# Kernel tuning notes

Measured on AMD Instinct MI355X. Metric: run time of the kernel, lower is better.

## Reference

```python
import jax, jax.numpy as jnp
import numpy as np

SCALE_FACTORS = (0.5, 1.0)
ITERATIONS = (2, 2)
TAU = (1.0, 1.0)
SIGMA = (1.0, 1.0)
SIGMA_CUTOFF = 3.0
EPS = 1e-9
DHW = ('NCDHW', 'OIDHW', 'NCDHW')


def gaussian_kernel1d(sigma):
    radius = int(round(sigma * SIGMA_CUTOFF))
    x = np.arange(-radius, radius + 1, dtype=np.float32)
    k = np.exp(-0.5 * (x / sigma) ** 2)
    return jnp.asarray(k / k.sum())


def smooth3d(vf, kernel):
    # separable depthwise Gaussian over the 3 spatial axes; vf: (B,C,D,H,W)
    C = vf.shape[1]
    n = kernel.shape[0]
    for axis in range(3):
        shape = [1, 1, 1]
        shape[axis] = n
        kern = jnp.broadcast_to(kernel.reshape(1, 1, *shape), (C, 1, *shape))
        vf = jax.lax.conv_general_dilated(vf, kern, (1, 1, 1), 'SAME',
                                          feature_group_count=C, dimension_numbers=DHW)
    return vf


def resize_tri(x, spatial):
    return jax.image.resize(x, x.shape[:2] + tuple(spatial), method='trilinear')


def warp(img, flow):
    # trilinear grid-sample with voxel-space displacement, border clamping
    B, C, D, H, W = img.shape
    gz, gy, gx = jnp.meshgrid(jnp.arange(D, dtype=img.dtype),
                              jnp.arange(H, dtype=img.dtype),
                              jnp.arange(W, dtype=img.dtype), indexing='ij')
    base = jnp.stack([gz, gy, gx])  # (3,D,H,W)

    def one(im, fl):
        z = jnp.clip(base[0] + fl[0], 0.0, D - 1)
        y = jnp.clip(base[1] + fl[1], 0.0, H - 1)
        x = jnp.clip(base[2] + fl[2], 0.0, W - 1)
        z0 = jnp.floor(z); y0 = jnp.floor(y); x0 = jnp.floor(x)
        wz = z - z0; wy = y - y0; wx = x - x0
        z0i = z0.astype(jnp.int32); y0i = y0.astype(jnp.int32); x0i = x0.astype(jnp.int32)
        z1i = jnp.minimum(z0i + 1, D - 1)
        y1i = jnp.minimum(y0i + 1, H - 1)
        x1i = jnp.minimum(x0i + 1, W - 1)

        def g(zi, yi, xi):
            return im[:, zi, yi, xi]  # (C,D,H,W)

        return (g(z0i, y0i, x0i) * (1 - wz) * (1 - wy) * (1 - wx)
                + g(z0i, y0i, x1i) * (1 - wz) * (1 - wy) * wx
                + g(z0i, y1i, x0i) * (1 - wz) * wy * (1 - wx)
                + g(z0i, y1i, x1i) * (1 - wz) * wy * wx
                + g(z1i, y0i, x0i) * wz * (1 - wy) * (1 - wx)
                + g(z1i, y0i, x1i) * wz * (1 - wy) * wx
                + g(z1i, y1i, x0i) * wz * wy * (1 - wx)
                + g(z1i, y1i, x1i) * wz * wy * wx)

    return jax.vmap(one)(img, flow)


def demon_forces(warped, fixed):
    # 'active' demon forces: gradient of the warped moving image
    diff = warped - fixed                                  # (B,1,D,H,W)
    g = jnp.stack(jnp.gradient(warped[:, 0], axis=(1, 2, 3)), axis=1)  # (B,3,D,H,W)
    denom = jnp.sum(g * g, axis=1, keepdims=True) + diff * diff + EPS
    return diff * g / denom


def conv3(x, w, b=None):
    y = jax.lax.conv_general_dilated(x, w, (1, 1, 1), 'SAME', dimension_numbers=DHW)
    return y if b is None else y + b.reshape(1, -1, 1, 1, 1)


def inorm(x):  # InstanceNorm3d, affine=False, eps=1e-5
    m = x.mean(axis=(2, 3, 4), keepdims=True)
    v = x.var(axis=(2, 3, 4), keepdims=True)
    return (x - m) * jax.lax.rsqrt(v + 1e-5)


def mish(x):
    return x * jnp.tanh(jax.nn.softplus(x))


def updater(x, w1, w2, w3, w4, b4):
    x = mish(inorm(conv3(x, w1)))
    x = mish(inorm(conv3(x, w2)))
    x = mish(inorm(conv3(x, w3)))
    return conv3(x, w4, b4)


def match_vf(vf, spatial):
    old = vf.shape[2:]
    if tuple(old) == tuple(spatial):
        return vf
    vf2 = resize_tri(vf, spatial)
    scale = jnp.array([s1 / s2 for s1, s2 in zip(spatial, old)], dtype=vf.dtype)
    return vf2 * scale.reshape(1, 3, 1, 1, 1)


def registration(image, moving, w1, w2, w3, w4, b4):
    vf = None
    for i, (sf, iters) in enumerate(zip(SCALE_FACTORS, ITERATIONS)):
        spatial = tuple(int(s * sf) for s in image.shape[2:])
        si = resize_tri(image, spatial)
        smov = resize_tri(moving, spatial)
        vf = jnp.zeros((image.shape[0], 3) + spatial, image.dtype) if vf is None else match_vf(vf, spatial)
        kernel = gaussian_kernel1d(SIGMA[i]).astype(image.dtype)
        for _ in range(iters):
            warped = warp(smov, vf)
            forces = demon_forces(warped, si)
            feat = jnp.concatenate([forces, si, warped], axis=1)  # 5 channels
            vf = vf + TAU[i] * updater(feat, w1, w2, w3, w4, b4)
            vf = smooth3d(vf, kernel)
    vf = match_vf(vf, image.shape[2:])
    warped_full = warp(moving, vf)
    return warped_full, vf


def setup_inputs() -> dict:
    key = jax.random.key(0)
    ks = jax.random.split(key, 8)
    D = H = W = 96
    return {
        'image': jax.random.uniform(ks[0], (1, 1, D, H, W), jnp.float32),
        'mask': jnp.ones((1, 1, D, H, W), jnp.float32),
        'moving': jax.random.uniform(ks[1], (1, 1, D, H, W), jnp.float32),
        'spacing': jnp.ones((3,), jnp.float32),
        'w1': jax.random.normal(ks[2], (32, 5, 3, 3, 3), jnp.float32) * 0.05,
        'w2': jax.random.normal(ks[3], (64, 32, 3, 3, 3), jnp.float32) * 0.05,
        'w3': jax.random.normal(ks[4], (32, 64, 3, 3, 3), jnp.float32) * 0.05,
        'w4': jax.random.normal(ks[5], (3, 32, 3, 3, 3), jnp.float32) * 0.05,
        'b4': jnp.zeros((3,), jnp.float32),
    }


def reference(image, mask, moving, spacing, w1, w2, w3, w4, b4):
    # mask only feeds metrics/early-stopping (disabled: early_stopping_fn='none');
    # spacing unused since use_image_spacing=False.
    return registration(image, moving, w1, w2, w3, w4, b4)
```

## Files before the change

### kernel.cpp

```cpp
#include <hip/hip_runtime.h>
#include <hip/hip_bf16.h>


#define DEV __device__ __forceinline__
typedef __hip_bfloat16 bf16;
typedef __attribute__((ext_vector_type(8))) short short8;
typedef __attribute__((ext_vector_type(4))) float f32x4;

DEV float bfu(unsigned int u) {
  union { unsigned int i; float f; } x; x.i = u << 16; return x.f;
}
DEV unsigned short fbf(float f) {
  __hip_bfloat16 h = __float2bfloat16(f);
  return __builtin_bit_cast(unsigned short, h);
}

DEV float mishf(float v) {
  if (v > 20.f) return v;
  float u = __expf(v);
  float w = u * (u + 2.f);
  return v * (w / (w + 2.f));
}

__global__ void zero_k(float* __restrict__ p, int n) {
  int i = blockIdx.x * 256 + threadIdx.x;
  if (i < n) p[i] = 0.f;
}
__global__ void copy_k(const float* __restrict__ in, float* __restrict__ out, int n) {
  int i = blockIdx.x * 256 + threadIdx.x;
  if (i < n) out[i] = in[i];
}

__global__ void pack_wf_k(const float* __restrict__ w, bf16* __restrict__ dst,
                          int NWT, int KB, int COR, int CIR) {
  int idx = blockIdx.x * 256 + threadIdx.x;
  int tot = 27 * NWT * KB * 512;
  if (idx >= tot) return;
  int j = idx & 7;
  int lane = (idx >> 3) & 63;
  int frag = idx >> 9;
  int kb = frag % KB;
  int r2 = frag / KB;
  int nwt = r2 % NWT;
  int off = r2 / NWT;
  int co = nwt * 16 + (lane & 15);
  int ci = (kb * 4 + (lane >> 4)) * 8 + j;
  float v = (co < COR && ci < CIR) ? w[((size_t)co * CIR + ci) * 27 + off] : 0.f;
  dst[idx] = __float2bfloat16(v);
}

DEV int ds_taps(int i, int n_out, int* j0, float* w) {
  if (i == 0) { *j0 = 0; w[0] = 3.f/7.f; w[1] = 3.f/7.f; w[2] = 1.f/7.f; return 3; }
  if (i == n_out - 1) { *j0 = 2*i - 1; w[0] = 1.f/7.f; w[1] = 3.f/7.f; w[2] = 3.f/7.f; return 3; }
  *j0 = 2*i - 1; w[0] = 0.125f; w[1] = 0.375f; w[2] = 0.375f; w[3] = 0.125f; return 4;
}
DEV void up_taps(int i, int n_in, int* j0, int* j1, float* w0, float* w1) {
  if (i & 1) {
    int k = i >> 1;
    if (k + 1 >= n_in) { *j0 = n_in - 1; *j1 = n_in - 1; *w0 = 1.f; *w1 = 0.f; }
    else { *j0 = k; *j1 = k + 1; *w0 = 0.75f; *w1 = 0.25f; }
  } else {
    int k = i >> 1;
    if (k == 0) { *j0 = 0; *j1 = 0; *w0 = 1.f; *w1 = 0.f; }
    else { *j0 = k - 1; *j1 = k; *w0 = 0.25f; *w1 = 0.75f; }
  }
}

__global__ void down2x_k(const float* __restrict__ in, float* __restrict__ out,
                         int Do, int Ho, int Wo) {
  const int Hi = 2 * Ho, Wi = 2 * Wo;
  const int No = Do * Ho * Wo;
  int i = blockIdx.x * 256 + threadIdx.x;
  if (i >= No) return;
  int xo = i % Wo; int t = i / Wo; int yo = t % Ho; int zo = t / Ho;
  int jz0, jy0, jx0; float wz[4], wy[4], wx[4];
  int cz = ds_taps(zo, Do, &jz0, wz);
  int cy = ds_taps(yo, Ho, &jy0, wy);
  int cx = ds_taps(xo, Wo, &jx0, wx);
  float s = 0.f;
  for (int a = 0; a < cz; ++a) {
    const float* pz = in + (size_t)(jz0 + a) * Hi * Wi;
    for (int b = 0; b < cy; ++b) {
      const float* py = pz + (size_t)(jy0 + b) * Wi;
      float wab = wz[a] * wy[b];
      for (int d = 0; d < cx; ++d) s += wab * wx[d] * py[jx0 + d];
    }
  }
  out[i] = s;
}

__global__ void up2x_vf_k(const float* __restrict__ in, float* __restrict__ out,
                          int Do, int Ho, int Wo) {
  const int Di = Do / 2, Hi = Ho / 2, Wi = Wo / 2;
  const int No = Do * Ho * Wo;
  const int c = blockIdx.y;
  int i = blockIdx.x * 256 + threadIdx.x;
  if (i >= No) return;
  int xo = i % Wo; int t = i / Wo; int yo = t % Ho; int zo = t / Ho;
  int jz0, jz1, jy0, jy1, jx0, jx1; float wz0, wz1, wy0, wy1, wx0, wx1;
  up_taps(zo, Di, &jz0, &jz1, &wz0, &wz1);
  up_taps(yo, Hi, &jy0, &jy1, &wy0, &wy1);
  up_taps(xo, Wi, &jx0, &jx1, &wx0, &wx1);
  const float* p = in + (size_t)c * Di * Hi * Wi;
  float v00 = wx0 * p[(jz0 * Hi + jy0) * Wi + jx0] + wx1 * p[(jz0 * Hi + jy0) * Wi + jx1];
  float v01 = wx0 * p[(jz0 * Hi + jy1) * Wi + jx0] + wx1 * p[(jz0 * Hi + jy1) * Wi + jx1];
  float v10 = wx0 * p[(jz1 * Hi + jy0) * Wi + jx0] + wx1 * p[(jz1 * Hi + jy0) * Wi + jx1];
  float v11 = wx0 * p[(jz1 * Hi + jy1) * Wi + jx0] + wx1 * p[(jz1 * Hi + jy1) * Wi + jx1];
  float s = wz0 * (wy0 * v00 + wy1 * v01) + wz1 * (wy0 * v10 + wy1 * v11);
  out[(size_t)c * No + i] = 2.f * s;
}

DEV float warp1(const float* __restrict__ img, const float* __restrict__ vf,
                int x, int y, int z, size_t i, int D, int H, int W, size_t N) {
  float zc = fminf(fmaxf((float)z + vf[i], 0.f), (float)(D - 1));
  float yc = fminf(fmaxf((float)y + vf[N + i], 0.f), (float)(H - 1));
  float xc = fminf(fmaxf((float)x + vf[2 * N + i], 0.f), (float)(W - 1));
  float zf = floorf(zc), yf = floorf(yc), xf = floorf(xc);
  int z0 = (int)zf, y0 = (int)yf, x0 = (int)xf;
  float wz = zc - zf, wy = yc - yf, wx = xc - xf;
  int z1 = min(z0 + 1, D - 1), y1 = min(y0 + 1, H - 1), x1 = min(x0 + 1, W - 1);
  const int HW = H * W;
  float v000 = img[z0 * HW + y0 * W + x0];
  float v001 = img[z0 * HW + y0 * W + x1];
  float v010 = img[z0 * HW + y1 * W + x0];
  float v011 = img[z0 * HW + y1 * W + x1];
  float v100 = img[z1 * HW + y0 * W + x0];
  float v101 = img[z1 * HW + y0 * W + x1];
  float v110 = img[z1 * HW + y1 * W + x0];
  float v111 = img[z1 * HW + y1 * W + x1];
  return v000 * (1 - wz) * (1 - wy) * (1 - wx)
       + v001 * (1 - wz) * (1 - wy) * wx
       + v010 * (1 - wz) * wy * (1 - wx)
       + v011 * (1 - wz) * wy * wx
       + v100 * wz * (1 - wy) * (1 - wx)
       + v101 * wz * (1 - wy) * wx
       + v110 * wz * wy * (1 - wx)
       + v111 * wz * wy * wx;
}

__global__ void warp_k(const float* __restrict__ img, const float* __restrict__ vf,
                       float* __restrict__ out, int D, int H, int W) {
  const size_t N = (size_t)D * H * W;
  size_t i = (size_t)blockIdx.x * 256 + threadIdx.x;
  if (i >= N) return;
  int x = i % W; int t = i / W; int y = t % H; int z = t / H;
  out[i] = warp1(img, vf, x, y, z, i, D, H, W, N);
}

__global__ void __launch_bounds__(256) warpforce_k(
    const float* __restrict__ img, const float* __restrict__ vf,
    const float* __restrict__ si, bf16* __restrict__ feat, int D, int H, int W) {
  __shared__ float wt[600];
  const size_t N = (size_t)D * H * W;
  const int t = threadIdx.x;
  const int tx = t & 7, ty = (t >> 3) & 7, tz = t >> 6;
  const int gx0 = blockIdx.x * 8, gy0 = blockIdx.y * 8, gz0 = blockIdx.z * 4;
  for (int cid = t; cid < 600; cid += 256) {
    int hx = cid % 10; int r = cid / 10; int hy = r % 10; int hz = r / 10;
    int gz = gz0 + hz - 1, gy = gy0 + hy - 1, gx = gx0 + hx - 1;
    float w = 0.f;
    if (((unsigned)gz < (unsigned)D) & ((unsigned)gy < (unsigned)H) & ((unsigned)gx < (unsigned)W)) {
      size_t i = (size_t)(gz * H + gy) * W + gx;
      w = warp1(img, vf, gx, gy, gz, i, D, H, W, N);
    }
    wt[cid] = w;
  }
  __syncthreads();
  const int x = gx0 + tx, y = gy0 + ty, z = gz0 + tz;
  const size_t i = (size_t)(z * H + y) * W + x;
  const int c = (tz + 1) * 100 + (ty + 1) * 10 + (tx + 1);
  float wv = wt[c];
  float gz = (z == 0) ? (wt[c + 100] - wv) : (z == D - 1) ? (wv - wt[c - 100]) : 0.5f * (wt[c + 100] - wt[c - 100]);
  float gy = (y == 0) ? (wt[c + 10] - wv) : (y == H - 1) ? (wv - wt[c - 10]) : 0.5f * (wt[c + 10] - wt[c - 10]);
  float gx = (x == 0) ? (wt[c + 1] - wv) : (x == W - 1) ? (wv - wt[c - 1]) : 0.5f * (wt[c + 1] - wt[c - 1]);
  float s = si[i];
  float diff = wv - s;
  float denom = gz * gz + gy * gy + gx * gx + diff * diff + 1e-9f;
  short8 o;
  o[0] = (short)fbf((diff * gz) / denom);
  o[1] = (short)fbf((diff * gy) / denom);
  o[2] = (short)fbf((diff * gx) / denom);
  o[3] = (short)fbf(s);
  o[4] = (short)fbf(wv);
  o[5] = 0; o[6] = 0; o[7] = 0;
  *(short8*)((short*)feat + i * 8) = o;
}

template <int CIN, int COUT, int TZ, int TY, int INS, int REDUCE>
__global__ void __launch_bounds__(512) convmf_k(
    const bf16* __restrict__ act, const bf16* __restrict__ wpk,
    bf16* __restrict__ out, double* __restrict__ pbuf, int D, int H, int W) {
  constexpr int CH = CIN / 8;
  constexpr int HZ = TZ + 2, HY = TY + 2;
  constexpr int HALO = HZ * HY * 18;
  constexpr int MS = TZ * TY / 4;
  constexpr int NS = COUT / 32;
  constexpr int NWT = COUT / 16;
  constexpr int KB = CIN / 32;
  __shared__ short lds[HALO * CIN];
  __shared__ float2 red[8][NS][16];
  const int t = threadIdx.x;
  const int gx0 = blockIdx.x * 16, gy0 = blockIdx.y * TY, gz0 = blockIdx.z * TZ;
  const short* actS = (const short*)act;
  for (int cid = t; cid < HALO * CH; cid += 512) {
    int pos = cid / CH, c = cid - pos * CH;
    int hx = pos % 18; int r = pos / 18; int hy = r % HY; int hz = r / HY;
    int gz = gz0 + hz - 1, gy = gy0 + hy - 1, gx = gx0 + hx - 1;
    uint4 v = {0u, 0u, 0u, 0u};
    if (((unsigned)gz < (unsigned)D) & ((unsigned)gy < (unsigned)H) & ((unsigned)gx < (unsigned)W)) {
      size_t vox = (size_t)(gz * H + gy) * W + gx;
      if (INS == 8) { if (c == 0) v = *(const uint4*)(actS + vox * 8); }
      else v = *(const uint4*)(actS + vox * CIN + c * 8);
    }
    *(uint4*)(lds + pos * CIN + ((c ^ (pos & (CH - 1))) * 8)) = v;
  }
  __syncthreads();
  const int lane = t & 63, wid = t >> 6;
  const int mw = wid & 3, nw = wid >> 2;
  const int lid = lane & 15, kg = lane >> 4;
  f32x4 acc[MS][NS];
#pragma unroll
  for (int ms = 0; ms < MS; ++ms)
#pragma unroll
    for (int n = 0; n < NS; ++n) acc[ms][n] = {0.f, 0.f, 0.f, 0.f};
  int rowpos[MS];
#pragma unroll
  for (int ms = 0; ms < MS; ++ms) {
    int r = mw * MS + ms;
    rowpos[ms] = ((r / TY) * HY + (r % TY)) * 18 + lid;
  }
  const short* wp = (const short*)wpk;
#pragma unroll 1
  for (int kz = 0; kz < 3; ++kz)
#pragma unroll 1
    for (int ky = 0; ky < 3; ++ky) {
      const int delta0 = (kz * HY + ky) * 18;
#pragma unroll
      for (int kx = 0; kx < 3; ++kx) {
        const int off = (kz * 3 + ky) * 3 + kx;
        short8 bq[NS][KB];
#pragma unroll
        for (int n = 0; n < NS; ++n)
#pragma unroll
          for (int kb = 0; kb < KB; ++kb)
            bq[n][kb] = *(const short8*)(wp + ((((size_t)off * NWT + nw * NS + n) * KB + kb) << 9) + lane * 8);
#pragma unroll
        for (int ms = 0; ms < MS; ++ms) {
          int pos = rowpos[ms] + delta0 + kx;
          int sw = pos & (CH - 1);
#pragma unroll
          for (int kb = 0; kb < KB; ++kb) {
            short8 a = *(const short8*)(lds + pos * CIN + (((kb * 4 + kg) ^ sw) * 8));
#pragma unroll
            for (int n = 0; n < NS; ++n)
              acc[ms][n] = __builtin_amdgcn_mfma_f32_16x16x32_bf16(a, bq[n][kb], acc[ms][n], 0, 0, 0);
          }
        }
      }
    }
  const int xe = kg * 4;
#pragma unroll
  for (int ms = 0; ms < MS; ++ms) {
    int r = mw * MS + ms;
    int z = gz0 + r / TY, y = gy0 + r % TY;
    size_t voxb = (size_t)(z * H + y) * W + gx0;
#pragma unroll
    for (int n = 0; n < NS; ++n) {
      int co = nw * NS * 16 + n * 16 + lid;
#pragma unroll
      for (int rg = 0; rg < 4; ++rg)
        out[(voxb + xe + rg) * COUT + co] = __float2bfloat16(acc[ms][n][rg]);
    }
  }
  if (REDUCE) {
#pragma unroll
    for (int n = 0; n < NS; ++n) {
      float s = 0.f, q = 0.f;
#pragma unroll
      for (int ms = 0; ms < MS; ++ms)
#pragma unroll
        for (int rg = 0; rg < 4; ++rg) {
          float v = acc[ms][n][rg];
          s += v; q += v * v;
        }
      s += __shfl_xor(s, 16); q += __shfl_xor(q, 16);
      s += __shfl_xor(s, 32); q += __shfl_xor(q, 32);
      if (lane < 16) red[wid][n][lane] = make_float2(s, q);
    }
    __syncthreads();
    if (t < COUT) {
      const int nw_ = t / (NS * 16);
      const int rem = t - nw_ * NS * 16;
      const int n_ = rem >> 4, lid_ = rem & 15;
      float S = 0.f, Q = 0.f;
#pragma unroll
      for (int m = 0; m < 4; ++m) {
        float2 v = red[nw_ * 4 + m][n_][lid_];
        S += v.x; Q += v.y;
      }
      const int G = gridDim.x * gridDim.y * gridDim.z;
      const int bid = blockIdx.x + gridDim.x * (blockIdx.y + gridDim.y * blockIdx.z);
      pbuf[((size_t)t * G + bid) * 2 + 0] = (double)S;
      pbuf[((size_t)t * G + bid) * 2 + 1] = (double)Q;
    }
  }
}

template <int TZ, int TY>
__global__ void __launch_bounds__(512) conv4mf_k(
    const bf16* __restrict__ act, const bf16* __restrict__ wpk,
    const float* __restrict__ bias, float* __restrict__ vf, int D, int H, int W) {
  constexpr int CH = 4;
  constexpr int HZ = TZ + 2, HY = TY + 2;
  constexpr int HALO = HZ * HY * 18;
  constexpr int MS = TZ * TY / 8;
  __shared__ short lds[HALO * 32];
  const int t = threadIdx.x;
  const int gx0 = blockIdx.x * 16, gy0 = blockIdx.y * TY, gz0 = blockIdx.z * TZ;
  const int N = D * H * W;
  const short* actS = (const short*)act;
  for (int cid = t; cid < HALO * CH; cid += 512) {
    int pos = cid / CH, c = cid - pos * CH;
    int hx = pos % 18; int r = pos / 18; int hy = r % HY; int hz = r / HY;
    int gz = gz0 + hz - 1, gy = gy0 + hy - 1, gx = gx0 + hx - 1;
    uint4 v = {0u, 0u, 0u, 0u};
    if (((unsigned)gz < (unsigned)D) & ((unsigned)gy < (unsigned)H) & ((unsigned)gx < (unsigned)W))
      v = *(const uint4*)(actS + ((size_t)(gz * H + gy) * W + gx) * 32 + c * 8);
    *(uint4*)(lds + pos * 32 + ((c ^ (pos & 3)) * 8)) = v;
  }
  __syncthreads();
  const int lane = t & 63, wid = t >> 6;
  const int lid = lane & 15, kg = lane >> 4;
  f32x4 acc[MS];
#pragma unroll
  for (int ms = 0; ms < MS; ++ms) acc[ms] = {0.f, 0.f, 0.f, 0.f};
  int rowpos[MS];
#pragma unroll
  for (int ms = 0; ms < MS; ++ms) {
    int r = wid * MS + ms;
    rowpos[ms] = ((r / TY) * HY + (r % TY)) * 18 + lid;
  }
  const short* wp = (const short*)wpk;
#pragma unroll 1
  for (int kz = 0; kz < 3; ++kz)
#pragma unroll 1
    for (int ky = 0; ky < 3; ++ky) {
      const int delta0 = (kz * HY + ky) * 18;
#pragma unroll
      for (int kx = 0; kx < 3; ++kx) {
        const int off = (kz * 3 + ky) * 3 + kx;
        short8 b = *(const short8*)(wp + ((size_t)off << 9) + lane * 8);
#pragma unroll
        for (int ms = 0; ms < MS; ++ms) {
          int pos = rowpos[ms] + delta0 + kx;
          int sw = pos & 3;
          short8 a = *(const short8*)(lds + pos * 32 + ((kg ^ sw) * 8));
          acc[ms] = __builtin_amdgcn_mfma_f32_16x16x32_bf16(a, b, acc[ms], 0, 0, 0);
        }
      }
    }
  if (lid < 3) {
    float bs = bias[lid];
#pragma unroll
    for (int ms = 0; ms < MS; ++ms) {
      int r = wid * MS + ms;
      int z = gz0 + r / TY, y = gy0 + r % TY;
      size_t voxb = (size_t)(z * H + y) * W + gx0 + kg * 4;
      float* p = vf + (size_t)lid * N + voxb;
#pragma unroll
      for (int rg = 0; rg < 4; ++rg) p[rg] += acc[ms][rg] + bs;
    }
  }
}

__global__ void stage2_k(const double* __restrict__ pbuf, float2* __restrict__ musc,
                         int N, int G) {
  const int c = blockIdx.x;
  double S = 0, Q = 0;
  for (int g = threadIdx.x; g < G; g += 256) {
    S += pbuf[((size_t)c * G + g) * 2 + 0];
    Q += pbuf[((size_t)c * G + g) * 2 + 1];
  }
  for (int off = 32; off > 0; off >>= 1) {
    S += __shfl_down(S, off); Q += __shfl_down(Q, off);
  }
  __shared__ double ls[4], lq[4];
  const int wid = threadIdx.x >> 6, lane = threadIdx.x & 63;
  if (lane == 0) { ls[wid] = S; lq[wid] = Q; }
  __syncthreads();
  if (threadIdx.x == 0) {
    double St = ls[0] + ls[1] + ls[2] + ls[3];
    double Qt = lq[0] + lq[1] + lq[2] + lq[3];
    double m = St / N;
    double var = Qt / N - m * m;
    musc[c] = make_float2((float)m, (float)(1.0 / sqrt(var + 1e-5)));
  }
}

template <int C>
__global__ void inorm_vc_k(bf16* __restrict__ x, const float2* __restrict__ musc, int N) {
  constexpr int CP = C / 2;
  constexpr int VPB = 256 / CP;
  const int cp = threadIdx.x & (CP - 1);
  const int vt = threadIdx.x / CP;
  float2 m0 = musc[2 * cp], m1 = musc[2 * cp + 1];
  unsigned int* p = (unsigned int*)x;
  int v0 = blockIdx.x * (4 * VPB) + vt;
#pragma unroll
  for (int r = 0; r < 4; ++r) {
    int v = v0 + r * VPB;
    size_t idx = (size_t)v * CP + cp;
    unsigned int u = p[idx];
    float a = mishf((bfu(u & 0xffffu) - m0.x) * m0.y);
    float b = mishf((bfu(u >> 16) - m1.x) * m1.y);
    p[idx] = (unsigned int)fbf(a) | ((unsigned int)fbf(b) << 16);
  }
}

template <int AXIS>
__global__ void smooth_k(const float* __restrict__ in, float* __restrict__ out,
                         int D, int H, int W) {
  const int N = D * H * W;
  const int c = blockIdx.y;
  int i = blockIdx.x * 256 + threadIdx.x;
  if (i >= N) return;
  int x = i % W; int t = i / W; int y = t % H; int z = t / H;
  const int coord = AXIS == 0 ? z : AXIS == 1 ? y : x;
  const int len = AXIS == 0 ? D : AXIS == 1 ? H : W;
  const int stride = AXIS == 0 ? H * W : AXIS == 1 ? W : 1;
  const float k1 = 0.60653065971263342f, k2 = 0.13533528323661270f, k3 = 0.011108996538242306f;
  const float kn = 1.f / (1.f + 2.f * (k1 + k2 + k3));
  const float gw[4] = {kn, k1 * kn, k2 * kn, k3 * kn};
  const float* p = in + (size_t)c * N;
  float s = gw[0] * p[i];
#pragma unroll
  for (int tt = 1; tt <= 3; ++tt) {
    if (coord - tt >= 0) s += gw[tt] * p[i - tt * stride];
    if (coord + tt < len) s += gw[tt] * p[i + tt * stride];
  }
  out[(size_t)c * N + i] = s;
}

extern "C" void kernel_launch(void* const* d_in, const int* in_sizes, int n_in,
                              void* d_out, int out_size, void* d_ws, size_t ws_size,
                              hipStream_t stream) {
  const float* image  = (const float*)d_in[0];
  const float* moving = (const float*)d_in[2];
  const float* w1 = (const float*)d_in[4];
  const float* w2 = (const float*)d_in[5];
  const float* w3 = (const float*)d_in[6];
  const float* w4 = (const float*)d_in[7];
  const float* b4 = (const float*)d_in[8];
  float* out = (float*)d_out;

  const int D1 = 96; const int N1 = D1 * D1 * D1;
  const int D0 = 48; const int N0 = D0 * D0 * D0;

  char* wsp = (char*)d_ws;
  double* pbuf  = (double*)wsp;          wsp += (size_t)64 * 13824 * 2 * 8;
  float2* musc  = (float2*)wsp;          wsp += 1024;
  bf16* w1p     = (bf16*)wsp;            wsp += 27 * 2 * 1 * 512 * 2;
  bf16* w2p     = (bf16*)wsp;            wsp += 27 * 4 * 1 * 512 * 2;
  bf16* w3p     = (bf16*)wsp;            wsp += 27 * 2 * 2 * 512 * 2;
  bf16* w4p     = (bf16*)wsp;            wsp += 27 * 1 * 1 * 512 * 2;
  float* si0    = (float*)wsp;           wsp += (size_t)N0 * 4;
  float* smov0  = (float*)wsp;           wsp += (size_t)N0 * 4;
  float* vf0    = (float*)wsp;           wsp += 3 * (size_t)N1 * 4;
  float* vf1    = (float*)wsp;           wsp += 3 * (size_t)N1 * 4;
  bf16* feat    = (bf16*)wsp;            wsp += 8 * (size_t)N1 * 2;
  bf16* bufA    = (bf16*)wsp;            wsp += 32 * (size_t)N1 * 2;
  bf16* bufB    = (bf16*)wsp;            wsp += 64 * (size_t)N1 * 2;

  pack_wf_k<<<(27 * 2 * 512 + 255) / 256, 256, 0, stream>>>(w1, w1p, 2, 1, 32, 5);
  pack_wf_k<<<(27 * 4 * 512 + 255) / 256, 256, 0, stream>>>(w2, w2p, 4, 1, 64, 32);
  pack_wf_k<<<(27 * 4 * 512 + 255) / 256, 256, 0, stream>>>(w3, w3p, 2, 2, 32, 64);
  pack_wf_k<<<(27 * 1 * 512 + 255) / 256, 256, 0, stream>>>(w4, w4p, 1, 1, 3, 32);

  down2x_k<<<N0 / 256, 256, 0, stream>>>(image, si0, D0, D0, D0);
  down2x_k<<<N0 / 256, 256, 0, stream>>>(moving, smov0, D0, D0, D0);
  zero_k<<<3 * N0 / 256, 256, 0, stream>>>(vf0, 3 * N0);

  float* vfc = vf0;
  float* vfa = vf1;

  auto run_level = [&](const float* si, const float* smov, int Dd) {
    const int N = Dd * Dd * Dd;
    const int nb = N / 256;
    const dim3 gw(Dd / 8, Dd / 8, Dd / 4);
    const dim3 g1(Dd / 16, Dd / 4, Dd / 4);
    const dim3 g3(Dd / 16, Dd / 4, Dd / 2);
    const int G1 = g1.x * g1.y * g1.z;
    const int G3 = g3.x * g3.y * g3.z;
    for (int it = 0; it < 2; ++it) {
      warpforce_k<<<gw, 256, 0, stream>>>(smov, vfc, si, feat, Dd, Dd, Dd);

      convmf_k<32, 32, 4, 4, 8, 1><<<g1, 512, 0, stream>>>(feat, w1p, bufA, pbuf, Dd, Dd, Dd);
      stage2_k<<<32, 256, 0, stream>>>(pbuf, musc, N, G1);
      inorm_vc_k<32><<<N / 64, 256, 0, stream>>>(bufA, musc, N);

      convmf_k<32, 64, 4, 4, 32, 1><<<g1, 512, 0, stream>>>(bufA, w2p, bufB, pbuf, Dd, Dd, Dd);
      stage2_k<<<64, 256, 0, stream>>>(pbuf, musc, N, G1);
      inorm_vc_k<64><<<N / 32, 256, 0, stream>>>(bufB, musc, N);

      convmf_k<64, 32, 2, 4, 64, 1><<<g3, 512, 0, stream>>>(bufB, w3p, bufA, pbuf, Dd, Dd, Dd);
      stage2_k<<<32, 256, 0, stream>>>(pbuf, musc, N, G3);
      inorm_vc_k<32><<<N / 64, 256, 0, stream>>>(bufA, musc, N);

      conv4mf_k<4, 4><<<g1, 512, 0, stream>>>(bufA, w4p, b4, vfc, Dd, Dd, Dd);

      smooth_k<0><<<dim3(nb, 3), 256, 0, stream>>>(vfc, vfa, Dd, Dd, Dd);
      smooth_k<1><<<dim3(nb, 3), 256, 0, stream>>>(vfa, vfc, Dd, Dd, Dd);
      smooth_k<2><<<dim3(nb, 3), 256, 0, stream>>>(vfc, vfa, Dd, Dd, Dd);
      { float* tmp = vfc; vfc = vfa; vfa = tmp; }
    }
  };

  run_level(si0, smov0, D0);

  up2x_vf_k<<<dim3(N1 / 256, 3), 256, 0, stream>>>(vfc, vfa, D1, D1, D1);
  { float* tmp = vfc; vfc = vfa; vfa = tmp; }

  run_level(image, moving, D1);

  warp_k<<<N1 / 256, 256, 0, stream>>>(moving, vfc, out, D1, D1, D1);
  copy_k<<<3 * N1 / 256, 256, 0, stream>>>(vfc, out + N1, 3 * N1);
}
```

Before: 1.358 ms.

## Pack conv1 taps into MFMA K dimension instead of padded channels

Adds a dedicated first-layer conv kernel that puts four 3D kernel taps into each 32-wide MFMA K slice, with 8 channels per tap (5 real). The old path padded the 5 input channels to 32 and ran 27 MFMA steps per output tile. The new path needs 7. This is meant to remove the wasted zero-padded MFMA work and the oversized LDS halo for the first conv. Weights are repacked to match the new layout. The last round clamps tap 27 to 26 and relies on zeroed weights for the padding.

```diff
diff --git a/kernel.cpp b/kernel.cpp
--- a/kernel.cpp
+++ b/kernel.cpp
@@ -46,6 +46,20 @@
   int co = nwt * 16 + (lane & 15);
   int ci = (kb * 4 + (lane >> 4)) * 8 + j;
   float v = (co < COR && ci < CIR) ? w[((size_t)co * CIR + ci) * 27 + off] : 0.f;
+  dst[idx] = __float2bfloat16(v);
+}
+
+__global__ void pack_w1p_k(const float* __restrict__ w, bf16* __restrict__ dst) {
+  int idx = blockIdx.x * 256 + threadIdx.x;
+  if (idx >= 7 * 2 * 512) return;
+  int j = idx & 7;
+  int lane = (idx >> 3) & 63;
+  int frag = idx >> 9;
+  int nw = frag & 1;
+  int rd = frag >> 1;
+  int co = nw * 16 + (lane & 15);
+  int tap = rd * 4 + (lane >> 4);
+  float v = (tap < 27 && j < 5) ? w[((size_t)co * 5 + j) * 27 + tap] : 0.f;
   dst[idx] = __float2bfloat16(v);
 }
 
@@ -186,6 +200,93 @@
   *(short8*)((short*)feat + i * 8) = o;
 }
 
+template <int TZ, int TY>
+__global__ void __launch_bounds__(512) conv1p_k(
+    const bf16* __restrict__ feat, const bf16* __restrict__ wpk,
+    bf16* __restrict__ out, double* __restrict__ pbuf, int D, int H, int W) {
+  constexpr int HZ = TZ + 2, HY = TY + 2;
+  constexpr int HALO = HZ * HY * 18;
+  constexpr int MS = TZ * TY / 4;
+  __shared__ short lds[HALO * 8];
+  __shared__ float2 red[8][1][16];
+  const int t = threadIdx.x;
+  const int gx0 = blockIdx.x * 16, gy0 = blockIdx.y * TY, gz0 = blockIdx.z * TZ;
+  const short* featS = (const short*)feat;
+  for (int pos = t; pos < HALO; pos += 512) {
+    int hx = pos % 18; int r = pos / 18; int hy = r % HY; int hz = r / HY;
+    int gz = gz0 + hz - 1, gy = gy0 + hy - 1, gx = gx0 + hx - 1;
+    uint4 v = {0u, 0u, 0u, 0u};
+    if (((unsigned)gz < (unsigned)D) & ((unsigned)gy < (unsigned)H) & ((unsigned)gx < (unsigned)W))
+      v = *(const uint4*)(featS + ((size_t)(gz * H + gy) * W + gx) * 8);
+    *(uint4*)(lds + pos * 8) = v;
+  }
+  __syncthreads();
+  const int lane = t & 63, wid = t >> 6;
+  const int mw = wid & 3, nw = wid >> 2;
+  const int lid = lane & 15, kg = lane >> 4;
+  f32x4 acc[MS];
+#pragma unroll
+  for (int ms = 0; ms < MS; ++ms) acc[ms] = {0.f, 0.f, 0.f, 0.f};
+  int rowpos[MS];
+#pragma unroll
+  for (int ms = 0; ms < MS; ++ms) {
+    int r = mw * MS + ms;
+    rowpos[ms] = ((r / TY) * HY + (r % TY)) * 18 + lid;
+  }
+  const short* wp = (const short*)wpk;
+#pragma unroll
+  for (int rd = 0; rd < 7; ++rd) {
+    int tap = rd * 4 + kg;
+    int tp = tap > 26 ? 26 : tap;
+    int kz = tp / 9, ky = (tp / 3) % 3, kx = tp % 3;
+    int delta = (kz * HY + ky) * 18 + kx;
+    short8 b = *(const short8*)(wp + ((size_t)(rd * 2 + nw) << 9) + lane * 8);
+#pragma unroll
+    for (int ms = 0; ms < MS; ++ms) {
+      short8 a = *(const short8*)(lds + (rowpos[ms] + delta) * 8);
+      acc[ms] = __builtin_amdgcn_mfma_f32_16x16x32_bf16(a, b, acc[ms], 0, 0, 0);
+    }
+  }
+  const int xe = kg * 4;
+#pragma unroll
+  for (int ms = 0; ms < MS; ++ms) {
+    int r = mw * MS + ms;
+    int z = gz0 + r / TY, y = gy0 + r % TY;
+    size_t voxb = (size_t)(z * H + y) * W + gx0;
+    int co = nw * 16 + lid;
+#pragma unroll
+    for (int rg = 0; rg < 4; ++rg)
+      out[(voxb + xe + rg) * 32 + co] = __float2bfloat16(acc[ms][rg]);
+  }
+  {
+    float s = 0.f, q = 0.f;
+#pragma unroll
+    for (int ms = 0; ms < MS; ++ms)
+#pragma unroll
+      for (int rg = 0; rg < 4; ++rg) {
+        float v = acc[ms][rg];
+        s += v; q += v * v;
+      }
+    s += __shfl_xor(s, 16); q += __shfl_xor(q, 16);
+    s += __shfl_xor(s, 32); q += __shfl_xor(q, 32);
+    if (lane < 16) red[wid][0][lane] = make_float2(s, q);
+    __syncthreads();
+    if (t < 32) {
+      const int nw_ = t >> 4, lid_ = t & 15;
+      float S = 0.f, Q = 0.f;
+#pragma unroll
+      for (int m = 0; m < 4; ++m) {
+        float2 v = red[nw_ * 4 + m][0][lid_];
+        S += v.x; Q += v.y;
+      }
+      const int G = gridDim.x * gridDim.y * gridDim.z;
+      const int bid = blockIdx.x + gridDim.x * (blockIdx.y + gridDim.y * blockIdx.z);
+      pbuf[((size_t)t * G + bid) * 2 + 0] = (double)S;
+      pbuf[((size_t)t * G + bid) * 2 + 1] = (double)Q;
+    }
+  }
+}
+
 template <int CIN, int COUT, int TZ, int TY, int INS, int REDUCE>
 __global__ void __launch_bounds__(512) convmf_k(
     const bf16* __restrict__ act, const bf16* __restrict__ wpk,
@@ -471,7 +572,7 @@
   bf16* bufA    = (bf16*)wsp;            wsp += 32 * (size_t)N1 * 2;
   bf16* bufB    = (bf16*)wsp;            wsp += 64 * (size_t)N1 * 2;
 
-  pack_wf_k<<<(27 * 2 * 512 + 255) / 256, 256, 0, stream>>>(w1, w1p, 2, 1, 32, 5);
+  pack_w1p_k<<<(7 * 2 * 512 + 255) / 256, 256, 0, stream>>>(w1, w1p);
   pack_wf_k<<<(27 * 4 * 512 + 255) / 256, 256, 0, stream>>>(w2, w2p, 4, 1, 64, 32);
   pack_wf_k<<<(27 * 4 * 512 + 255) / 256, 256, 0, stream>>>(w3, w3p, 2, 2, 32, 64);
   pack_wf_k<<<(27 * 1 * 512 + 255) / 256, 256, 0, stream>>>(w4, w4p, 1, 1, 3, 32);
@@ -494,7 +595,7 @@
     for (int it = 0; it < 2; ++it) {
       warpforce_k<<<gw, 256, 0, stream>>>(smov, vfc, si, feat, Dd, Dd, Dd);
 
-      convmf_k<32, 32, 4, 4, 8, 1><<<g1, 512, 0, stream>>>(feat, w1p, bufA, pbuf, Dd, Dd, Dd);
+      conv1p_k<4, 4><<<g1, 512, 0, stream>>>(feat, w1p, bufA, pbuf, Dd, Dd, Dd);
       stage2_k<<<32, 256, 0, stream>>>(pbuf, musc, N, G1);
       inorm_vc_k<32><<<N / 64, 256, 0, stream>>>(bufA, musc, N);
 
```

New measurement: 1.271 ms. -6.4%, faster.
